# Optimization experiments

Measured on AMD Instinct MI355X. Metric: run time of the kernel, lower is better.

Reference implementation:

```python
import jax, jax.numpy as jnp
import numpy as np

B, NC, D, C, HM = 4096, 32, 128, 256, 2
H = HM * D
EPS = 1e-5


def _ln(x, g, b):
    mu = jnp.mean(x, axis=-1, keepdims=True)
    var = jnp.mean(jnp.square(x - mu), axis=-1, keepdims=True)
    return (x - mu) * jax.lax.rsqrt(var + EPS) * g + b


def setup_inputs() -> dict:
    key = jax.random.key(0)
    ks = jax.random.split(key, 16)
    s = 0.05
    return {
        "cx": jax.random.normal(ks[0], (B, 16), jnp.float32),
        "cat_vecs": jax.random.normal(ks[1], (B, NC, D), jnp.float32),
        "embed_weights": jax.random.normal(ks[2], (NC, C, D), jnp.float32),
        "Wq": jax.random.normal(ks[3], (NC, D, D), jnp.float32) * s,
        "Wk": jax.random.normal(ks[4], (NC, D, D), jnp.float32) * s,
        "Wv": jax.random.normal(ks[5], (NC, D, D), jnp.float32) * s,
        "ln1_g": jnp.ones((D,), jnp.float32),
        "ln1_b": jnp.zeros((D,), jnp.float32),
        "W1": jax.random.normal(ks[6], (NC, D, H), jnp.float32) * s,
        "b1": jnp.zeros((NC, H), jnp.float32),
        "W2": jax.random.normal(ks[7], (NC, H, D), jnp.float32) * s,
        "b2": jnp.zeros((NC, D), jnp.float32),
        "ln2_g": jnp.ones((D,), jnp.float32),
        "ln2_b": jnp.zeros((D,), jnp.float32),
        "Ws": jax.random.normal(ks[8], (NC, D), jnp.float32) * s,
        "bs": jnp.zeros((NC,), jnp.float32),
    }


def reference(cx, cat_vecs, embed_weights, Wq, Wk, Wv, ln1_g, ln1_b, W1, b1, W2, b2, ln2_g, ln2_b, Ws, bs):
    # cx is unused by the original forward body.
    # Per-feature projections, batched over the Nc axis (j).
    q = jnp.einsum('bjd,jde->bje', cat_vecs, Wq)          # [B, Nc, D]
    k = jnp.einsum('jcd,jde->jce', embed_weights, Wk)     # [Nc, C, D]
    v = jnp.einsum('jcd,jde->jce', embed_weights, Wv)     # [Nc, C, D]
    scores = jnp.einsum('bjd,jcd->bjc', q, k) / jnp.sqrt(jnp.asarray(D, q.dtype))
    alpha = jax.nn.softmax(scores, axis=-1)               # [B, Nc, C]
    h = jnp.einsum('bjc,jcd->bjd', alpha, v)              # [B, Nc, D]
    h = _ln(cat_vecs + h, ln1_g, ln1_b)
    ff = jnp.einsum('bjd,jdh->bjh', h, W1) + b1
    ff = jnp.einsum('bjh,jhd->bjd', jax.nn.relu(ff), W2) + b2
    h = _ln(h + ff, ln2_g, ln2_b)
    out = jax.nn.sigmoid(jnp.einsum('bjd,jd->bj', h, Ws) + bs)  # [B, Nc]
    return out
```

## Files before the change

kernel.cpp:

```cpp
#include <hip/hip_runtime.h>


typedef __attribute__((ext_vector_type(4))) float f32x4;
typedef __attribute__((ext_vector_type(8))) short bf16x8;
typedef __attribute__((ext_vector_type(4))) unsigned u32x4;

#define DEVI static __device__ __forceinline__
#define SB __builtin_amdgcn_sched_barrier(0)
#define BARR __builtin_amdgcn_s_barrier()
#define MEMF asm volatile("" ::: "memory")

constexpr int NC = 32, D = 128, C = 256, H = 256;

DEVI unsigned short f2b(float f) {
  unsigned u = __builtin_bit_cast(unsigned, f);
  u += 0x7fffu + ((u >> 16) & 1u);
  return (unsigned short)(u >> 16);
}
DEVI float b2f(unsigned short h) {
  unsigned u = ((unsigned)h) << 16;
  return __builtin_bit_cast(float, u);
}
DEVI unsigned pk2(float a, float b) {
  return (unsigned)f2b(a) | ((unsigned)f2b(b) << 16);
}
DEVI unsigned cvtpk(float a, float b) {
  unsigned r;
  asm("v_cvt_pk_bf16_f32 %0, %1, %2" : "=v"(r) : "v"(a), "v"(b));
  return r;
}

template <int N> DEVI void vmwait() {
  asm volatile("s_waitcnt vmcnt(%0)" ::"n"(N) : "memory");
}
DEVI void lgkm0() { asm volatile("s_waitcnt lgkmcnt(0)" ::: "memory"); }

DEVI void gload16(const void* g, void* l) {
  __builtin_amdgcn_global_load_lds(
      (const __attribute__((address_space(1))) void*)g,
      (__attribute__((address_space(3))) void*)l, 16, 0, 0);
}


__global__ __launch_bounds__(256) void prepA_kernel(
    const float* __restrict__ emb, const float* __restrict__ Wk,
    const float* __restrict__ Wv, const float* __restrict__ W1,
    const float* __restrict__ W2, float* __restrict__ Ktmp,
    unsigned short* __restrict__ VtP, unsigned short* __restrict__ W1tP,
    unsigned short* __restrict__ W2tP) {
  __shared__ __align__(16) float smem[20480];
  const int bid = blockIdx.x, tid = threadIdx.x;
  if (bid < 512) {
    const bool isV = bid >= 256;
    const int bb = isV ? bid - 256 : bid;
    const int j = bb >> 3, ct = bb & 7;
    float* wm = smem;
    float* eb = smem + 16384;
    const float4* gw = (const float4*)((isV ? Wv : Wk) + (long)j * D * D);
    float4* lw = (float4*)wm;
    for (int i = tid; i < D * D / 4; i += 256) lw[i] = gw[i];
    const float4* ge = (const float4*)(emb + ((long)j * C + ct * 32) * D);
    float4* le = (float4*)eb;
    for (int i = tid; i < 32 * D / 4; i += 256) le[i] = ge[i];
    __syncthreads();
    const int e = tid & 127, h = tid >> 7;
    float acc[16];
#pragma unroll
    for (int r = 0; r < 16; ++r) acc[r] = 0.f;
    for (int d = 0; d < D; ++d) {
      float wde = wm[d * 128 + e];
#pragma unroll
      for (int r = 0; r < 16; ++r)
        acc[r] = fmaf(eb[(h * 16 + r) * 128 + d], wde, acc[r]);
    }
    if (!isV) {
      for (int r = 0; r < 16; ++r)
        Ktmp[((long)j * C + ct * 32 + h * 16 + r) * D + e] = acc[r];
    } else {
#pragma unroll
      for (int k = 0; k < 2; ++k) {
        uint4 pk = {pk2(acc[k * 8 + 0], acc[k * 8 + 1]),
                    pk2(acc[k * 8 + 2], acc[k * 8 + 3]),
                    pk2(acc[k * 8 + 4], acc[k * 8 + 5]),
                    pk2(acc[k * 8 + 6], acc[k * 8 + 7])};
        int slot = ct * 4 + h * 2 + k;
        long byte = (long)j * 65536 + e * 512 + ((slot ^ (e & 7)) << 4);
        *(uint4*)((char*)VtP + byte) = pk;
      }
    }
  } else {
    float(*t)[33] = reinterpret_cast<float(*)[33]>(smem);
    const int idx = bid - 512;
    const bool isW2 = idx >= 1024;
    const int bb = isW2 ? idx - 1024 : idx;
    const int j = bb >> 5, tile = bb & 31;
    const int rr = tid >> 3, c4 = tid & 7;
    if (!isW2) {
      const int dt = tile & 3, ht = tile >> 2;
      float4 v = *(const float4*)(W1 + ((long)j * 128 + dt * 32 + rr) * 256 + ht * 32 + c4 * 4);
      t[rr][c4 * 4 + 0] = v.x; t[rr][c4 * 4 + 1] = v.y;
      t[rr][c4 * 4 + 2] = v.z; t[rr][c4 * 4 + 3] = v.w;
      __syncthreads();
      int row = ht * 32 + rr, colb = dt * 32 + c4 * 4;
      uint2 pk = {pk2(t[c4 * 4 + 0][rr], t[c4 * 4 + 1][rr]),
                  pk2(t[c4 * 4 + 2][rr], t[c4 * 4 + 3][rr])};
      long byte = (long)j * 65536 + row * 256 + (((colb >> 3) ^ (row & 7)) << 4) + (colb & 7) * 2;
      *(uint2*)((char*)W1tP + byte) = pk;
    } else {
      const int et = tile & 3, ht = tile >> 2;
      float4 v = *(const float4*)(W2 + ((long)j * 256 + ht * 32 + rr) * 128 + et * 32 + c4 * 4);
      t[rr][c4 * 4 + 0] = v.x; t[rr][c4 * 4 + 1] = v.y;
      t[rr][c4 * 4 + 2] = v.z; t[rr][c4 * 4 + 3] = v.w;
      __syncthreads();
      int row = et * 32 + rr, colb = ht * 32 + c4 * 4;
      uint2 pk = {pk2(t[c4 * 4 + 0][rr], t[c4 * 4 + 1][rr]),
                  pk2(t[c4 * 4 + 2][rr], t[c4 * 4 + 3][rr])};
      long byte = (long)j * 65536 + row * 512 + (((colb >> 3) ^ (row & 7)) << 4) + (colb & 7) * 2;
      *(uint2*)((char*)W2tP + byte) = pk;
    }
  }
}

__global__ __launch_bounds__(256) void prepB_kernel(
    const float* __restrict__ Wq, const float* __restrict__ Ktmp,
    unsigned short* __restrict__ MtP) {
  __shared__ float wqT[128][68];
  __shared__ float kt[32][129];
  const int bid = blockIdx.x;
  const int j = bid >> 4, ct = (bid >> 1) & 7, dh = bid & 1;
  const int tid = threadIdx.x;
  for (int i = tid; i < 64 * 32; i += 256) {
    int dloc = i >> 5, e4 = i & 31;
    float4 v = *(const float4*)(Wq + ((long)j * 128 + dh * 64 + dloc) * 128 + e4 * 4);
    wqT[e4 * 4 + 0][dloc] = v.x; wqT[e4 * 4 + 1][dloc] = v.y;
    wqT[e4 * 4 + 2][dloc] = v.z; wqT[e4 * 4 + 3][dloc] = v.w;
  }
  for (int i = tid; i < 32 * 32; i += 256) {
    int r = i >> 5, c0 = (i & 31) * 4;
    float4 v = *(const float4*)(Ktmp + ((long)j * 256 + ct * 32 + r) * 128 + c0);
    kt[r][c0 + 0] = v.x; kt[r][c0 + 1] = v.y;
    kt[r][c0 + 2] = v.z; kt[r][c0 + 3] = v.w;
  }
  __syncthreads();
  const int cl = tid >> 3, s = tid & 7;
  float acc[8];
#pragma unroll
  for (int u = 0; u < 8; ++u) acc[u] = 0.f;
  for (int e = 0; e < 128; ++e) {
    float kk = kt[cl][e];
    float4 a = *(const float4*)&wqT[e][s * 8];
    float4 b = *(const float4*)&wqT[e][s * 8 + 4];
    acc[0] = fmaf(a.x, kk, acc[0]); acc[1] = fmaf(a.y, kk, acc[1]);
    acc[2] = fmaf(a.z, kk, acc[2]); acc[3] = fmaf(a.w, kk, acc[3]);
    acc[4] = fmaf(b.x, kk, acc[4]); acc[5] = fmaf(b.y, kk, acc[5]);
    acc[6] = fmaf(b.z, kk, acc[6]); acc[7] = fmaf(b.w, kk, acc[7]);
  }
  const float scale = 0.08838834764831845f;
  int c = ct * 32 + cl;
  uint4 pk = {pk2(acc[0] * scale, acc[1] * scale),
              pk2(acc[2] * scale, acc[3] * scale),
              pk2(acc[4] * scale, acc[5] * scale),
              pk2(acc[6] * scale, acc[7] * scale)};
  int slot = dh * 8 + s;
  long byte = (long)j * 65536 + c * 256 + ((slot ^ (c & 7)) << 4);
  *(uint4*)((char*)MtP + byte) = pk;
}

__global__ __launch_bounds__(256, 4) void fused_kernel(
    const float* __restrict__ x, const unsigned short* __restrict__ MtP,
    const unsigned short* __restrict__ VtP, const unsigned short* __restrict__ W1tP,
    const unsigned short* __restrict__ W2tP, const float* __restrict__ b1,
    const float* __restrict__ b2, const float* __restrict__ g1,
    const float* __restrict__ be1, const float* __restrict__ g2,
    const float* __restrict__ be2, const float* __restrict__ Ws,
    const float* __restrict__ bs, float* __restrict__ out) {
  __shared__ __align__(16) unsigned short wb[2][8192];
  __shared__ __align__(16) float sv[1024];
  const int bid = blockIdx.x;
  const int wg = (bid & 7) * 256 + (bid >> 3);
  const int j = wg >> 6, b0 = (wg & 63) * 64;
  const int tid = threadIdx.x, w = tid >> 6, l = tid & 63, lr = l & 15, lg = l >> 4;
  const int bloc = w * 16 + lr;

  const unsigned short* pnl0 = MtP + (long)j * 32768;
  const unsigned short* pnl1 = VtP + (long)j * 32768;
  const unsigned short* pnl2 = W1tP + (long)j * 32768;
  const unsigned short* pnl3 = W2tP + (long)j * 32768;

  auto ISSUE = [&](int s2) {
    const unsigned short* base = (s2 < 4) ? pnl0 : (s2 < 8) ? pnl1 : (s2 < 12) ? pnl2 : pnl3;
    const char* gq = (const char*)(base + (s2 & 3) * 8192);
    char* lb = (char*)&wb[s2 & 1][0] + w * 4096;
    SB;
#pragma unroll
    for (int t = 0; t < 4; ++t)
      gload16(gq + (w * 4 + t) * 1024 + l * 16, lb + t * 1024);
    SB;
  };

  const float* xrow = x + ((long)(b0 + bloc) * NC + j) * D;
  float4 xf[4][2];
#pragma unroll
  for (int kc = 0; kc < 4; ++kc) {
    xf[kc][0] = *(const float4*)(xrow + kc * 32 + lg * 8);
    xf[kc][1] = *(const float4*)(xrow + kc * 32 + lg * 8 + 4);
  }
  for (int i = tid; i < 1024; i += 256) {
    float v;
    if (i < 256) v = b1[j * H + i];
    else if (i < 384) v = b2[j * D + i - 256];
    else if (i < 512) v = g1[i - 384];
    else if (i < 640) v = be1[i - 512];
    else if (i < 768) v = g2[i - 640];
    else if (i < 896) v = be2[i - 768];
    else v = Ws[j * D + i - 896];
    sv[i] = v;
  }
  SB;
  ISSUE(0);
  ISSUE(1);
  float bsj = bs[j];
  bf16x8 xa[4];
#pragma unroll
  for (int kc = 0; kc < 4; ++kc) {
    u32x4 t;
    t[0] = cvtpk(xf[kc][0].x, xf[kc][0].y);
    t[1] = cvtpk(xf[kc][0].z, xf[kc][0].w);
    t[2] = cvtpk(xf[kc][1].x, xf[kc][1].y);
    t[3] = cvtpk(xf[kc][1].z, xf[kc][1].w);
    xa[kc] = __builtin_bit_cast(bf16x8, t);
  }
  lgkm0(); SB; BARR; MEMF; SB;

  int inner[4], inner2[8];
#pragma unroll
  for (int kc = 0; kc < 4; ++kc)
    inner[kc] = lr * 256 + (((kc * 4 + lg) ^ (lr & 7)) << 4);
#pragma unroll
  for (int kc = 0; kc < 8; ++kc)
    inner2[kc] = lr * 512 + (((kc * 4 + lg) ^ (lr & 7)) << 4);

  const int ad0 = (((lg & 1) << 5) + lr) << 2;
  const int ad1 = ad0 + 64;
  const bool hi = (lg >> 1) != 0;

  bf16x8 aa[8], xa2[4], aa2[8];
  unsigned hb[8][2];
  float4 xr[8];

  f32x4 sc[16];
#pragma unroll
  for (int t = 0; t < 16; ++t) sc[t] = (f32x4){0.f, 0.f, 0.f, 0.f};
#pragma unroll
  for (int q = 0; q < 4; ++q) {
    vmwait<4>(); SB; BARR; MEMF; SB;
    const char* wp = (const char*)wb[q & 1];
    __builtin_amdgcn_s_setprio(1);
#pragma unroll
    for (int c4 = 0; c4 < 4; ++c4)
#pragma unroll
      for (int kc = 0; kc < 4; ++kc) {
        bf16x8 bf = *(const bf16x8*)(wp + c4 * 4096 + inner[kc]);
        sc[q * 4 + c4] =
            __builtin_amdgcn_mfma_f32_16x16x32_bf16(bf, xa[kc], sc[q * 4 + c4], 0, 0, 0);
      }
    __builtin_amdgcn_s_setprio(0);
    if (q == 3) {
      float mx = -1e30f;
#pragma unroll
      for (int ct = 0; ct < 16; ++ct)
#pragma unroll
        for (int i = 0; i < 4; ++i) mx = fmaxf(mx, sc[ct][i]);
      mx = fmaxf(mx, __shfl_xor(mx, 16));
      mx = fmaxf(mx, __shfl_xor(mx, 32));
      float sm = 0.f;
#pragma unroll
      for (int ct = 0; ct < 16; ++ct)
#pragma unroll
        for (int i = 0; i < 4; ++i) {
          float e = __expf(sc[ct][i] - mx);
          sc[ct][i] = e;
          sm += e;
        }
      sm += __shfl_xor(sm, 16);
      sm += __shfl_xor(sm, 32);
      float inv = 1.f / sm;
      unsigned au[16][2];
#pragma unroll
      for (int ct = 0; ct < 16; ++ct) {
        au[ct][0] = cvtpk(sc[ct][0] * inv, sc[ct][1] * inv);
        au[ct][1] = cvtpk(sc[ct][2] * inv, sc[ct][3] * inv);
      }
#pragma unroll
      for (int kc = 0; kc < 8; ++kc) {
        u32x4 t;
#pragma unroll
        for (int h = 0; h < 2; ++h) {
          int ad = h ? ad1 : ad0;
#pragma unroll
          for (int p = 0; p < 2; ++p) {
            int f0 = __builtin_amdgcn_ds_bpermute(ad, (int)au[2 * kc][p]);
            int f1 = __builtin_amdgcn_ds_bpermute(ad, (int)au[2 * kc + 1][p]);
            t[h * 2 + p] = (unsigned)(hi ? f1 : f0);
          }
        }
        aa[kc] = __builtin_bit_cast(bf16x8, t);
      }
    }
    lgkm0(); SB; BARR; MEMF; SB;
    ISSUE(q + 2);
  }

  f32x4 ha[8];
#pragma unroll
  for (int t = 0; t < 8; ++t) ha[t] = (f32x4){0.f, 0.f, 0.f, 0.f};
#pragma unroll
  for (int q = 0; q < 4; ++q) {
    vmwait<4>(); SB; BARR; MEMF; SB;
    const char* wp = (const char*)wb[q & 1];
    __builtin_amdgcn_s_setprio(1);
#pragma unroll
    for (int e2 = 0; e2 < 2; ++e2)
#pragma unroll
      for (int kc = 0; kc < 8; ++kc) {
        bf16x8 bf = *(const bf16x8*)(wp + e2 * 8192 + inner2[kc]);
        ha[q * 2 + e2] =
            __builtin_amdgcn_mfma_f32_16x16x32_bf16(bf, aa[kc], ha[q * 2 + e2], 0, 0, 0);
      }
    __builtin_amdgcn_s_setprio(0);
    if (q == 2) {
#pragma unroll
      for (int et = 0; et < 8; ++et)
        xr[et] = *(const float4*)(xrow + et * 16 + lg * 4);
    }
    if (q == 3) {
      float hvv[8][4];
      float s1 = 0.f, s2s = 0.f;
#pragma unroll
      for (int et = 0; et < 8; ++et)
#pragma unroll
        for (int i = 0; i < 4; ++i) {
          float v = ha[et][i] + xr[et][i];
          hvv[et][i] = v;
          s1 += v;
          s2s += v * v;
        }
      s1 += __shfl_xor(s1, 16); s2s += __shfl_xor(s2s, 16);
      s1 += __shfl_xor(s1, 32); s2s += __shfl_xor(s2s, 32);
      float mu = s1 * (1.f / 128.f);
      float var = s2s * (1.f / 128.f) - mu * mu;
      float rs = rsqrtf(var + 1e-5f);
#pragma unroll
      for (int et = 0; et < 8; ++et) {
        f32x4 gg = *(const f32x4*)&sv[384 + et * 16 + lg * 4];
        f32x4 bb = *(const f32x4*)&sv[512 + et * 16 + lg * 4];
        float h0 = (hvv[et][0] - mu) * rs * gg[0] + bb[0];
        float h1n = (hvv[et][1] - mu) * rs * gg[1] + bb[1];
        float h2 = (hvv[et][2] - mu) * rs * gg[2] + bb[2];
        float h3 = (hvv[et][3] - mu) * rs * gg[3] + bb[3];
        hb[et][0] = cvtpk(h0, h1n);
        hb[et][1] = cvtpk(h2, h3);
      }
#pragma unroll
      for (int kc = 0; kc < 4; ++kc) {
        u32x4 t;
#pragma unroll
        for (int h = 0; h < 2; ++h) {
          int ad = h ? ad1 : ad0;
#pragma unroll
          for (int p = 0; p < 2; ++p) {
            int f0 = __builtin_amdgcn_ds_bpermute(ad, (int)hb[2 * kc][p]);
            int f1 = __builtin_amdgcn_ds_bpermute(ad, (int)hb[2 * kc + 1][p]);
            t[h * 2 + p] = (unsigned)(hi ? f1 : f0);
          }
        }
        xa2[kc] = __builtin_bit_cast(bf16x8, t);
      }
    }
    lgkm0(); SB; BARR; MEMF; SB;
    ISSUE(6 + q);
  }

  unsigned ffu[16][2];
#pragma unroll
  for (int q = 0; q < 4; ++q) {
    vmwait<4>(); SB; BARR; MEMF; SB;
    const char* wp = (const char*)wb[q & 1];
    f32x4 fa4[4];
#pragma unroll
    for (int t = 0; t < 4; ++t) fa4[t] = (f32x4){0.f, 0.f, 0.f, 0.f};
    __builtin_amdgcn_s_setprio(1);
#pragma unroll
    for (int c4 = 0; c4 < 4; ++c4)
#pragma unroll
      for (int kc = 0; kc < 4; ++kc) {
        bf16x8 bf = *(const bf16x8*)(wp + c4 * 4096 + inner[kc]);
        fa4[c4] =
            __builtin_amdgcn_mfma_f32_16x16x32_bf16(bf, xa2[kc], fa4[c4], 0, 0, 0);
      }
    __builtin_amdgcn_s_setprio(0);
#pragma unroll
    for (int c4 = 0; c4 < 4; ++c4) {
      int ht = q * 4 + c4;
      f32x4 bb = *(const f32x4*)&sv[ht * 16 + lg * 4];
      float v0 = fmaxf(fa4[c4][0] + bb[0], 0.f);
      float v1 = fmaxf(fa4[c4][1] + bb[1], 0.f);
      float v2 = fmaxf(fa4[c4][2] + bb[2], 0.f);
      float v3 = fmaxf(fa4[c4][3] + bb[3], 0.f);
      ffu[ht][0] = cvtpk(v0, v1);
      ffu[ht][1] = cvtpk(v2, v3);
    }
    if (q == 3) {
#pragma unroll
      for (int kc = 0; kc < 8; ++kc) {
        u32x4 t;
#pragma unroll
        for (int h = 0; h < 2; ++h) {
          int ad = h ? ad1 : ad0;
#pragma unroll
          for (int p = 0; p < 2; ++p) {
            int f0 = __builtin_amdgcn_ds_bpermute(ad, (int)ffu[2 * kc][p]);
            int f1 = __builtin_amdgcn_ds_bpermute(ad, (int)ffu[2 * kc + 1][p]);
            t[h * 2 + p] = (unsigned)(hi ? f1 : f0);
          }
        }
        aa2[kc] = __builtin_bit_cast(bf16x8, t);
      }
    }
    lgkm0(); SB; BARR; MEMF; SB;
    ISSUE(10 + q);
  }

  f32x4 oa[8];
#pragma unroll
  for (int t = 0; t < 8; ++t) oa[t] = (f32x4){0.f, 0.f, 0.f, 0.f};
#pragma unroll
  for (int q = 0; q < 4; ++q) {
    if (q == 3) { vmwait<0>(); } else { vmwait<4>(); }
    SB; BARR; MEMF; SB;
    const char* wp = (const char*)wb[q & 1];
    __builtin_amdgcn_s_setprio(1);
#pragma unroll
    for (int e2 = 0; e2 < 2; ++e2)
#pragma unroll
      for (int kc = 0; kc < 8; ++kc) {
        bf16x8 bf = *(const bf16x8*)(wp + e2 * 8192 + inner2[kc]);
        oa[q * 2 + e2] =
            __builtin_amdgcn_mfma_f32_16x16x32_bf16(bf, aa2[kc], oa[q * 2 + e2], 0, 0, 0);
      }
    __builtin_amdgcn_s_setprio(0);
    if (q < 3) {
      lgkm0(); SB; BARR; MEMF; SB;
      if (q < 2) ISSUE(14 + q);
    }
  }
  {
    float t1 = 0.f, t2 = 0.f;
#pragma unroll
    for (int et = 0; et < 8; ++et) {
      f32x4 bb = *(const f32x4*)&sv[256 + et * 16 + lg * 4];
      float r0 = b2f((unsigned short)(hb[et][0] & 0xffff));
      float r1 = b2f((unsigned short)(hb[et][0] >> 16));
      float r2 = b2f((unsigned short)(hb[et][1] & 0xffff));
      float r3 = b2f((unsigned short)(hb[et][1] >> 16));
      float v0 = oa[et][0] + bb[0] + r0;
      float v1 = oa[et][1] + bb[1] + r1;
      float v2 = oa[et][2] + bb[2] + r2;
      float v3 = oa[et][3] + bb[3] + r3;
      oa[et][0] = v0; oa[et][1] = v1; oa[et][2] = v2; oa[et][3] = v3;
      t1 += (v0 + v1) + (v2 + v3);
      t2 += (v0 * v0 + v1 * v1) + (v2 * v2 + v3 * v3);
    }
    t1 += __shfl_xor(t1, 16); t2 += __shfl_xor(t2, 16);
    t1 += __shfl_xor(t1, 32); t2 += __shfl_xor(t2, 32);
    float mu2 = t1 * (1.f / 128.f);
    float var = t2 * (1.f / 128.f) - mu2 * mu2;
    float rs2 = rsqrtf(var + 1e-5f);
    float lp = 0.f;
#pragma unroll
    for (int et = 0; et < 8; ++et) {
      f32x4 gg = *(const f32x4*)&sv[640 + et * 16 + lg * 4];
      f32x4 bb = *(const f32x4*)&sv[768 + et * 16 + lg * 4];
      f32x4 ww = *(const f32x4*)&sv[896 + et * 16 + lg * 4];
#pragma unroll
      for (int i = 0; i < 4; ++i) {
        float h2 = (oa[et][i] - mu2) * rs2 * gg[i] + bb[i];
        lp = fmaf(h2, ww[i], lp);
      }
    }
    lp += __shfl_xor(lp, 16);
    lp += __shfl_xor(lp, 32);
    if (lg == 0) {
      float sg = 1.f / (1.f + __expf(-(lp + bsj)));
      out[(long)(b0 + bloc) * NC + j] = sg;
    }
  }
}

extern "C" void kernel_launch(void* const* d_in, const int* in_sizes, int n_in,
                              void* d_out, int out_size, void* d_ws,
                              size_t ws_size, hipStream_t stream) {
  (void)in_sizes; (void)n_in; (void)out_size; (void)ws_size;
  const float* cat = (const float*)d_in[1];
  const float* emb = (const float*)d_in[2];
  const float* Wq = (const float*)d_in[3];
  const float* Wk = (const float*)d_in[4];
  const float* Wv = (const float*)d_in[5];
  const float* g1 = (const float*)d_in[6];
  const float* be1 = (const float*)d_in[7];
  const float* W1 = (const float*)d_in[8];
  const float* b1 = (const float*)d_in[9];
  const float* W2 = (const float*)d_in[10];
  const float* b2 = (const float*)d_in[11];
  const float* g2 = (const float*)d_in[12];
  const float* be2 = (const float*)d_in[13];
  const float* Ws = (const float*)d_in[14];
  const float* bs = (const float*)d_in[15];
  float* out = (float*)d_out;

  char* ws = (char*)d_ws;
  unsigned short* MtP = (unsigned short*)(ws);
  unsigned short* VtP = (unsigned short*)(ws + (2 << 20));
  unsigned short* W1tP = (unsigned short*)(ws + (4 << 20));
  unsigned short* W2tP = (unsigned short*)(ws + (6 << 20));
  float* Ktmp = (float*)(ws + (8 << 20));

  prepA_kernel<<<2560, 256, 0, stream>>>(emb, Wk, Wv, W1, W2, Ktmp, VtP, W1tP, W2tP);
  prepB_kernel<<<512, 256, 0, stream>>>(Wq, Ktmp, MtP);
  fused_kernel<<<2048, 256, 0, stream>>>(cat, MtP, VtP, W1tP, W2tP, b1, b2, g1,
                                         be1, g2, be2, Ws, bs, out);
}
```

Baseline: 114.3 us.

## Process two 64-row batch tiles per workgroup with continuous weight prefetch

Each workgroup now handles 128 batch rows for one feature j, as two sequential 64-row tiles, and the grid is halved. The weight-panel prefetch stream keeps running across the tile boundary, so the second tile's first panels load during the first tile's tail. This amortises launch and prologue cost and pipeline fill/drain per panel stream. The trade-off is fewer workgroups, which can reduce occupancy and load balance, and a serial dependency between the two tiles.

```diff
diff --git a/kernel.cpp b/kernel.cpp
--- a/kernel.cpp
+++ b/kernel.cpp
@@ -177,8 +177,8 @@
   __shared__ __align__(16) unsigned short wb[2][8192];
   __shared__ __align__(16) float sv[1024];
   const int bid = blockIdx.x;
-  const int wg = (bid & 7) * 256 + (bid >> 3);
-  const int j = wg >> 6, b0 = (wg & 63) * 64;
+  const int wg = (bid & 7) * 128 + (bid >> 3);
+  const int j = wg >> 5, bpair = wg & 31;
   const int tid = threadIdx.x, w = tid >> 6, l = tid & 63, lr = l & 15, lg = l >> 4;
   const int bloc = w * 16 + lr;
 
@@ -187,10 +187,11 @@
   const unsigned short* pnl2 = W1tP + (long)j * 32768;
   const unsigned short* pnl3 = W2tP + (long)j * 32768;
 
-  auto ISSUE = [&](int s2) {
-    const unsigned short* base = (s2 < 4) ? pnl0 : (s2 < 8) ? pnl1 : (s2 < 12) ? pnl2 : pnl3;
-    const char* gq = (const char*)(base + (s2 & 3) * 8192);
-    char* lb = (char*)&wb[s2 & 1][0] + w * 4096;
+  auto ISSUE = [&](int g) {
+    const int qq = g & 15;
+    const unsigned short* base = (qq < 4) ? pnl0 : (qq < 8) ? pnl1 : (qq < 12) ? pnl2 : pnl3;
+    const char* gq = (const char*)(base + (qq & 3) * 8192);
+    char* lb = (char*)&wb[g & 1][0] + w * 4096;
     SB;
 #pragma unroll
     for (int t = 0; t < 4; ++t)
@@ -198,7 +199,7 @@
     SB;
   };
 
-  const float* xrow = x + ((long)(b0 + bloc) * NC + j) * D;
+  const float* xrow = x + ((long)(bpair * 128 + bloc) * NC + j) * D;
   float4 xf[4][2];
 #pragma unroll
   for (int kc = 0; kc < 4; ++kc) {
@@ -244,255 +245,279 @@
   const int ad1 = ad0 + 64;
   const bool hi = (lg >> 1) != 0;
 
-  bf16x8 aa[8], xa2[4], aa2[8];
-  unsigned hb[8][2];
-  float4 xr[8];
-
-  f32x4 sc[16];
-#pragma unroll
-  for (int t = 0; t < 16; ++t) sc[t] = (f32x4){0.f, 0.f, 0.f, 0.f};
-#pragma unroll
-  for (int q = 0; q < 4; ++q) {
-    vmwait<4>(); SB; BARR; MEMF; SB;
-    const char* wp = (const char*)wb[q & 1];
-    __builtin_amdgcn_s_setprio(1);
-#pragma unroll
-    for (int c4 = 0; c4 < 4; ++c4)
+  for (int bt = 0; bt < 2; ++bt) {
+    const int b0 = bpair * 128 + bt * 64;
+    if (bt == 1) {
+      xrow = x + ((long)(b0 + bloc) * NC + j) * D;
 #pragma unroll
       for (int kc = 0; kc < 4; ++kc) {
-        bf16x8 bf = *(const bf16x8*)(wp + c4 * 4096 + inner[kc]);
-        sc[q * 4 + c4] =
-            __builtin_amdgcn_mfma_f32_16x16x32_bf16(bf, xa[kc], sc[q * 4 + c4], 0, 0, 0);
-      }
-    __builtin_amdgcn_s_setprio(0);
-    if (q == 3) {
-      float mx = -1e30f;
-#pragma unroll
-      for (int ct = 0; ct < 16; ++ct)
-#pragma unroll
-        for (int i = 0; i < 4; ++i) mx = fmaxf(mx, sc[ct][i]);
-      mx = fmaxf(mx, __shfl_xor(mx, 16));
-      mx = fmaxf(mx, __shfl_xor(mx, 32));
-      float sm = 0.f;
-#pragma unroll
-      for (int ct = 0; ct < 16; ++ct)
-#pragma unroll
-        for (int i = 0; i < 4; ++i) {
-          float e = __expf(sc[ct][i] - mx);
-          sc[ct][i] = e;
-          sm += e;
-        }
-      sm += __shfl_xor(sm, 16);
-      sm += __shfl_xor(sm, 32);
-      float inv = 1.f / sm;
-      unsigned au[16][2];
-#pragma unroll
-      for (int ct = 0; ct < 16; ++ct) {
-        au[ct][0] = cvtpk(sc[ct][0] * inv, sc[ct][1] * inv);
-        au[ct][1] = cvtpk(sc[ct][2] * inv, sc[ct][3] * inv);
-      }
-#pragma unroll
-      for (int kc = 0; kc < 8; ++kc) {
-        u32x4 t;
-#pragma unroll
-        for (int h = 0; h < 2; ++h) {
-          int ad = h ? ad1 : ad0;
-#pragma unroll
-          for (int p = 0; p < 2; ++p) {
-            int f0 = __builtin_amdgcn_ds_bpermute(ad, (int)au[2 * kc][p]);
-            int f1 = __builtin_amdgcn_ds_bpermute(ad, (int)au[2 * kc + 1][p]);
-            t[h * 2 + p] = (unsigned)(hi ? f1 : f0);
-          }
-        }
-        aa[kc] = __builtin_bit_cast(bf16x8, t);
-      }
-    }
-    lgkm0(); SB; BARR; MEMF; SB;
-    ISSUE(q + 2);
-  }
-
-  f32x4 ha[8];
-#pragma unroll
-  for (int t = 0; t < 8; ++t) ha[t] = (f32x4){0.f, 0.f, 0.f, 0.f};
-#pragma unroll
-  for (int q = 0; q < 4; ++q) {
-    vmwait<4>(); SB; BARR; MEMF; SB;
-    const char* wp = (const char*)wb[q & 1];
-    __builtin_amdgcn_s_setprio(1);
-#pragma unroll
-    for (int e2 = 0; e2 < 2; ++e2)
-#pragma unroll
-      for (int kc = 0; kc < 8; ++kc) {
-        bf16x8 bf = *(const bf16x8*)(wp + e2 * 8192 + inner2[kc]);
-        ha[q * 2 + e2] =
-            __builtin_amdgcn_mfma_f32_16x16x32_bf16(bf, aa[kc], ha[q * 2 + e2], 0, 0, 0);
-      }
-    __builtin_amdgcn_s_setprio(0);
-    if (q == 2) {
-#pragma unroll
-      for (int et = 0; et < 8; ++et)
-        xr[et] = *(const float4*)(xrow + et * 16 + lg * 4);
-    }
-    if (q == 3) {
-      float hvv[8][4];
-      float s1 = 0.f, s2s = 0.f;
-#pragma unroll
-      for (int et = 0; et < 8; ++et)
-#pragma unroll
-        for (int i = 0; i < 4; ++i) {
-          float v = ha[et][i] + xr[et][i];
-          hvv[et][i] = v;
-          s1 += v;
-          s2s += v * v;
-        }
-      s1 += __shfl_xor(s1, 16); s2s += __shfl_xor(s2s, 16);
-      s1 += __shfl_xor(s1, 32); s2s += __shfl_xor(s2s, 32);
-      float mu = s1 * (1.f / 128.f);
-      float var = s2s * (1.f / 128.f) - mu * mu;
-      float rs = rsqrtf(var + 1e-5f);
-#pragma unroll
-      for (int et = 0; et < 8; ++et) {
-        f32x4 gg = *(const f32x4*)&sv[384 + et * 16 + lg * 4];
-        f32x4 bb = *(const f32x4*)&sv[512 + et * 16 + lg * 4];
-        float h0 = (hvv[et][0] - mu) * rs * gg[0] + bb[0];
-        float h1n = (hvv[et][1] - mu) * rs * gg[1] + bb[1];
-        float h2 = (hvv[et][2] - mu) * rs * gg[2] + bb[2];
-        float h3 = (hvv[et][3] - mu) * rs * gg[3] + bb[3];
-        hb[et][0] = cvtpk(h0, h1n);
-        hb[et][1] = cvtpk(h2, h3);
-      }
+        xf[kc][0] = *(const float4*)(xrow + kc * 32 + lg * 8);
+        xf[kc][1] = *(const float4*)(xrow + kc * 32 + lg * 8 + 4);
+      }
+      vmwait<0>(); SB;
 #pragma unroll
       for (int kc = 0; kc < 4; ++kc) {
         u32x4 t;
-#pragma unroll
-        for (int h = 0; h < 2; ++h) {
-          int ad = h ? ad1 : ad0;
-#pragma unroll
-          for (int p = 0; p < 2; ++p) {
-            int f0 = __builtin_amdgcn_ds_bpermute(ad, (int)hb[2 * kc][p]);
-            int f1 = __builtin_amdgcn_ds_bpermute(ad, (int)hb[2 * kc + 1][p]);
-            t[h * 2 + p] = (unsigned)(hi ? f1 : f0);
+        t[0] = cvtpk(xf[kc][0].x, xf[kc][0].y);
+        t[1] = cvtpk(xf[kc][0].z, xf[kc][0].w);
+        t[2] = cvtpk(xf[kc][1].x, xf[kc][1].y);
+        t[3] = cvtpk(xf[kc][1].z, xf[kc][1].w);
+        xa[kc] = __builtin_bit_cast(bf16x8, t);
+      }
+    }
+    const int gb = bt * 16;
+
+    bf16x8 aa[8], xa2[4], aa2[8];
+    unsigned hb[8][2];
+    float4 xr[8];
+
+    f32x4 sc[16];
+#pragma unroll
+    for (int t = 0; t < 16; ++t) sc[t] = (f32x4){0.f, 0.f, 0.f, 0.f};
+#pragma unroll
+    for (int q = 0; q < 4; ++q) {
+      vmwait<4>(); SB; BARR; MEMF; SB;
+      const char* wp = (const char*)wb[q & 1];
+      __builtin_amdgcn_s_setprio(1);
+#pragma unroll
+      for (int c4 = 0; c4 < 4; ++c4)
+#pragma unroll
+        for (int kc = 0; kc < 4; ++kc) {
+          bf16x8 bf = *(const bf16x8*)(wp + c4 * 4096 + inner[kc]);
+          sc[q * 4 + c4] =
+              __builtin_amdgcn_mfma_f32_16x16x32_bf16(bf, xa[kc], sc[q * 4 + c4], 0, 0, 0);
+        }
+      __builtin_amdgcn_s_setprio(0);
+      if (q == 3) {
+        float mx = -1e30f;
+#pragma unroll
+        for (int ct = 0; ct < 16; ++ct)
+#pragma unroll
+          for (int i = 0; i < 4; ++i) mx = fmaxf(mx, sc[ct][i]);
+        mx = fmaxf(mx, __shfl_xor(mx, 16));
+        mx = fmaxf(mx, __shfl_xor(mx, 32));
+        float sm = 0.f;
+#pragma unroll
+        for (int ct = 0; ct < 16; ++ct)
+#pragma unroll
+          for (int i = 0; i < 4; ++i) {
+            float e = __expf(sc[ct][i] - mx);
+            sc[ct][i] = e;
+            sm += e;
           }
-        }
-        xa2[kc] = __builtin_bit_cast(bf16x8, t);
-      }
-    }
-    lgkm0(); SB; BARR; MEMF; SB;
-    ISSUE(6 + q);
-  }
-
-  unsigned ffu[16][2];
-#pragma unroll
-  for (int q = 0; q < 4; ++q) {
-    vmwait<4>(); SB; BARR; MEMF; SB;
-    const char* wp = (const char*)wb[q & 1];
-    f32x4 fa4[4];
-#pragma unroll
-    for (int t = 0; t < 4; ++t) fa4[t] = (f32x4){0.f, 0.f, 0.f, 0.f};
-    __builtin_amdgcn_s_setprio(1);
-#pragma unroll
-    for (int c4 = 0; c4 < 4; ++c4)
-#pragma unroll
-      for (int kc = 0; kc < 4; ++kc) {
-        bf16x8 bf = *(const bf16x8*)(wp + c4 * 4096 + inner[kc]);
-        fa4[c4] =
-            __builtin_amdgcn_mfma_f32_16x16x32_bf16(bf, xa2[kc], fa4[c4], 0, 0, 0);
-      }
-    __builtin_amdgcn_s_setprio(0);
-#pragma unroll
-    for (int c4 = 0; c4 < 4; ++c4) {
-      int ht = q * 4 + c4;
-      f32x4 bb = *(const f32x4*)&sv[ht * 16 + lg * 4];
-      float v0 = fmaxf(fa4[c4][0] + bb[0], 0.f);
-      float v1 = fmaxf(fa4[c4][1] + bb[1], 0.f);
-      float v2 = fmaxf(fa4[c4][2] + bb[2], 0.f);
-      float v3 = fmaxf(fa4[c4][3] + bb[3], 0.f);
-      ffu[ht][0] = cvtpk(v0, v1);
-      ffu[ht][1] = cvtpk(v2, v3);
-    }
-    if (q == 3) {
-#pragma unroll
-      for (int kc = 0; kc < 8; ++kc) {
-        u32x4 t;
-#pragma unroll
-        for (int h = 0; h < 2; ++h) {
-          int ad = h ? ad1 : ad0;
-#pragma unroll
-          for (int p = 0; p < 2; ++p) {
-            int f0 = __builtin_amdgcn_ds_bpermute(ad, (int)ffu[2 * kc][p]);
-            int f1 = __builtin_amdgcn_ds_bpermute(ad, (int)ffu[2 * kc + 1][p]);
-            t[h * 2 + p] = (unsigned)(hi ? f1 : f0);
+        sm += __shfl_xor(sm, 16);
+        sm += __shfl_xor(sm, 32);
+        float inv = 1.f / sm;
+        unsigned au[16][2];
+#pragma unroll
+        for (int ct = 0; ct < 16; ++ct) {
+          au[ct][0] = cvtpk(sc[ct][0] * inv, sc[ct][1] * inv);
+          au[ct][1] = cvtpk(sc[ct][2] * inv, sc[ct][3] * inv);
+        }
+#pragma unroll
+        for (int kc = 0; kc < 8; ++kc) {
+          u32x4 t;
+#pragma unroll
+          for (int h = 0; h < 2; ++h) {
+            int ad = h ? ad1 : ad0;
+#pragma unroll
+            for (int p = 0; p < 2; ++p) {
+              int f0 = __builtin_amdgcn_ds_bpermute(ad, (int)au[2 * kc][p]);
+              int f1 = __builtin_amdgcn_ds_bpermute(ad, (int)au[2 * kc + 1][p]);
+              t[h * 2 + p] = (unsigned)(hi ? f1 : f0);
+            }
           }
-        }
-        aa2[kc] = __builtin_bit_cast(bf16x8, t);
-      }
-    }
-    lgkm0(); SB; BARR; MEMF; SB;
-    ISSUE(10 + q);
-  }
-
-  f32x4 oa[8];
-#pragma unroll
-  for (int t = 0; t < 8; ++t) oa[t] = (f32x4){0.f, 0.f, 0.f, 0.f};
-#pragma unroll
-  for (int q = 0; q < 4; ++q) {
-    if (q == 3) { vmwait<0>(); } else { vmwait<4>(); }
-    SB; BARR; MEMF; SB;
-    const char* wp = (const char*)wb[q & 1];
-    __builtin_amdgcn_s_setprio(1);
-#pragma unroll
-    for (int e2 = 0; e2 < 2; ++e2)
-#pragma unroll
-      for (int kc = 0; kc < 8; ++kc) {
-        bf16x8 bf = *(const bf16x8*)(wp + e2 * 8192 + inner2[kc]);
-        oa[q * 2 + e2] =
-            __builtin_amdgcn_mfma_f32_16x16x32_bf16(bf, aa2[kc], oa[q * 2 + e2], 0, 0, 0);
-      }
-    __builtin_amdgcn_s_setprio(0);
-    if (q < 3) {
+          aa[kc] = __builtin_bit_cast(bf16x8, t);
+        }
+      }
       lgkm0(); SB; BARR; MEMF; SB;
-      if (q < 2) ISSUE(14 + q);
-    }
-  }
-  {
-    float t1 = 0.f, t2 = 0.f;
-#pragma unroll
-    for (int et = 0; et < 8; ++et) {
-      f32x4 bb = *(const f32x4*)&sv[256 + et * 16 + lg * 4];
-      float r0 = b2f((unsigned short)(hb[et][0] & 0xffff));
-      float r1 = b2f((unsigned short)(hb[et][0] >> 16));
-      float r2 = b2f((unsigned short)(hb[et][1] & 0xffff));
-      float r3 = b2f((unsigned short)(hb[et][1] >> 16));
-      float v0 = oa[et][0] + bb[0] + r0;
-      float v1 = oa[et][1] + bb[1] + r1;
-      float v2 = oa[et][2] + bb[2] + r2;
-      float v3 = oa[et][3] + bb[3] + r3;
-      oa[et][0] = v0; oa[et][1] = v1; oa[et][2] = v2; oa[et][3] = v3;
-      t1 += (v0 + v1) + (v2 + v3);
-      t2 += (v0 * v0 + v1 * v1) + (v2 * v2 + v3 * v3);
-    }
-    t1 += __shfl_xor(t1, 16); t2 += __shfl_xor(t2, 16);
-    t1 += __shfl_xor(t1, 32); t2 += __shfl_xor(t2, 32);
-    float mu2 = t1 * (1.f / 128.f);
-    float var = t2 * (1.f / 128.f) - mu2 * mu2;
-    float rs2 = rsqrtf(var + 1e-5f);
-    float lp = 0.f;
-#pragma unroll
-    for (int et = 0; et < 8; ++et) {
-      f32x4 gg = *(const f32x4*)&sv[640 + et * 16 + lg * 4];
-      f32x4 bb = *(const f32x4*)&sv[768 + et * 16 + lg * 4];
-      f32x4 ww = *(const f32x4*)&sv[896 + et * 16 + lg * 4];
-#pragma unroll
-      for (int i = 0; i < 4; ++i) {
-        float h2 = (oa[et][i] - mu2) * rs2 * gg[i] + bb[i];
-        lp = fmaf(h2, ww[i], lp);
-      }
-    }
-    lp += __shfl_xor(lp, 16);
-    lp += __shfl_xor(lp, 32);
-    if (lg == 0) {
-      float sg = 1.f / (1.f + __expf(-(lp + bsj)));
-      out[(long)(b0 + bloc) * NC + j] = sg;
+      ISSUE(gb + q + 2);
+    }
+
+    f32x4 ha[8];
+#pragma unroll
+    for (int t = 0; t < 8; ++t) ha[t] = (f32x4){0.f, 0.f, 0.f, 0.f};
+#pragma unroll
+    for (int q = 0; q < 4; ++q) {
+      vmwait<4>(); SB; BARR; MEMF; SB;
+      const char* wp = (const char*)wb[q & 1];
+      __builtin_amdgcn_s_setprio(1);
+#pragma unroll
+      for (int e2 = 0; e2 < 2; ++e2)
+#pragma unroll
+        for (int kc = 0; kc < 8; ++kc) {
+          bf16x8 bf = *(const bf16x8*)(wp + e2 * 8192 + inner2[kc]);
+          ha[q * 2 + e2] =
+              __builtin_amdgcn_mfma_f32_16x16x32_bf16(bf, aa[kc], ha[q * 2 + e2], 0, 0, 0);
+        }
+      __builtin_amdgcn_s_setprio(0);
+      if (q == 2) {
+#pragma unroll
+        for (int et = 0; et < 8; ++et)
+          xr[et] = *(const float4*)(xrow + et * 16 + lg * 4);
+      }
+      if (q == 3) {
+        float hvv[8][4];
+        float s1 = 0.f, s2s = 0.f;
+#pragma unroll
+        for (int et = 0; et < 8; ++et)
+#pragma unroll
+          for (int i = 0; i < 4; ++i) {
+            float v = ha[et][i] + xr[et][i];
+            hvv[et][i] = v;
+            s1 += v;
+            s2s += v * v;
+          }
+        s1 += __shfl_xor(s1, 16); s2s += __shfl_xor(s2s, 16);
+        s1 += __shfl_xor(s1, 32); s2s += __shfl_xor(s2s, 32);
+        float mu = s1 * (1.f / 128.f);
+        float var = s2s * (1.f / 128.f) - mu * mu;
+        float rs = rsqrtf(var + 1e-5f);
+#pragma unroll
+        for (int et = 0; et < 8; ++et) {
+          f32x4 gg = *(const f32x4*)&sv[384 + et * 16 + lg * 4];
+          f32x4 bb = *(const f32x4*)&sv[512 + et * 16 + lg * 4];
+          float h0 = (hvv[et][0] - mu) * rs * gg[0] + bb[0];
+          float h1n = (hvv[et][1] - mu) * rs * gg[1] + bb[1];
+          float h2 = (hvv[et][2] - mu) * rs * gg[2] + bb[2];
+          float h3 = (hvv[et][3] - mu) * rs * gg[3] + bb[3];
+          hb[et][0] = cvtpk(h0, h1n);
+          hb[et][1] = cvtpk(h2, h3);
+        }
+#pragma unroll
+        for (int kc = 0; kc < 4; ++kc) {
+          u32x4 t;
+#pragma unroll
+          for (int h = 0; h < 2; ++h) {
+            int ad = h ? ad1 : ad0;
+#pragma unroll
+            for (int p = 0; p < 2; ++p) {
+              int f0 = __builtin_amdgcn_ds_bpermute(ad, (int)hb[2 * kc][p]);
+              int f1 = __builtin_amdgcn_ds_bpermute(ad, (int)hb[2 * kc + 1][p]);
+              t[h * 2 + p] = (unsigned)(hi ? f1 : f0);
+            }
+          }
+          xa2[kc] = __builtin_bit_cast(bf16x8, t);
+        }
+      }
+      lgkm0(); SB; BARR; MEMF; SB;
+      ISSUE(gb + 6 + q);
+    }
+
+    unsigned ffu[16][2];
+#pragma unroll
+    for (int q = 0; q < 4; ++q) {
+      vmwait<4>(); SB; BARR; MEMF; SB;
+      const char* wp = (const char*)wb[q & 1];
+      f32x4 fa4[4];
+#pragma unroll
+      for (int t = 0; t < 4; ++t) fa4[t] = (f32x4){0.f, 0.f, 0.f, 0.f};
+      __builtin_amdgcn_s_setprio(1);
+#pragma unroll
+      for (int c4 = 0; c4 < 4; ++c4)
+#pragma unroll
+        for (int kc = 0; kc < 4; ++kc) {
+          bf16x8 bf = *(const bf16x8*)(wp + c4 * 4096 + inner[kc]);
+          fa4[c4] =
+              __builtin_amdgcn_mfma_f32_16x16x32_bf16(bf, xa2[kc], fa4[c4], 0, 0, 0);
+        }
+      __builtin_amdgcn_s_setprio(0);
+#pragma unroll
+      for (int c4 = 0; c4 < 4; ++c4) {
+        int ht = q * 4 + c4;
+        f32x4 bb = *(const f32x4*)&sv[ht * 16 + lg * 4];
+        float v0 = fmaxf(fa4[c4][0] + bb[0], 0.f);
+        float v1 = fmaxf(fa4[c4][1] + bb[1], 0.f);
+        float v2 = fmaxf(fa4[c4][2] + bb[2], 0.f);
+        float v3 = fmaxf(fa4[c4][3] + bb[3], 0.f);
+        ffu[ht][0] = cvtpk(v0, v1);
+        ffu[ht][1] = cvtpk(v2, v3);
+      }
+      if (q == 3) {
+#pragma unroll
+        for (int kc = 0; kc < 8; ++kc) {
+          u32x4 t;
+#pragma unroll
+          for (int h = 0; h < 2; ++h) {
+            int ad = h ? ad1 : ad0;
+#pragma unroll
+            for (int p = 0; p < 2; ++p) {
+              int f0 = __builtin_amdgcn_ds_bpermute(ad, (int)ffu[2 * kc][p]);
+              int f1 = __builtin_amdgcn_ds_bpermute(ad, (int)ffu[2 * kc + 1][p]);
+              t[h * 2 + p] = (unsigned)(hi ? f1 : f0);
+            }
+          }
+          aa2[kc] = __builtin_bit_cast(bf16x8, t);
+        }
+      }
+      lgkm0(); SB; BARR; MEMF; SB;
+      ISSUE(gb + 10 + q);
+    }
+
+    f32x4 oa[8];
+#pragma unroll
+    for (int t = 0; t < 8; ++t) oa[t] = (f32x4){0.f, 0.f, 0.f, 0.f};
+#pragma unroll
+    for (int q = 0; q < 4; ++q) {
+      if (bt == 1 && q == 3) { vmwait<0>(); } else { vmwait<4>(); }
+      SB; BARR; MEMF; SB;
+      const char* wp = (const char*)wb[q & 1];
+      __builtin_amdgcn_s_setprio(1);
+#pragma unroll
+      for (int e2 = 0; e2 < 2; ++e2)
+#pragma unroll
+        for (int kc = 0; kc < 8; ++kc) {
+          bf16x8 bf = *(const bf16x8*)(wp + e2 * 8192 + inner2[kc]);
+          oa[q * 2 + e2] =
+              __builtin_amdgcn_mfma_f32_16x16x32_bf16(bf, aa2[kc], oa[q * 2 + e2], 0, 0, 0);
+        }
+      __builtin_amdgcn_s_setprio(0);
+      if (q == 3) {
+        float t1 = 0.f, t2 = 0.f;
+#pragma unroll
+        for (int et = 0; et < 8; ++et) {
+          f32x4 bb = *(const f32x4*)&sv[256 + et * 16 + lg * 4];
+          float r0 = b2f((unsigned short)(hb[et][0] & 0xffff));
+          float r1 = b2f((unsigned short)(hb[et][0] >> 16));
+          float r2 = b2f((unsigned short)(hb[et][1] & 0xffff));
+          float r3 = b2f((unsigned short)(hb[et][1] >> 16));
+          float v0 = oa[et][0] + bb[0] + r0;
+          float v1 = oa[et][1] + bb[1] + r1;
+          float v2 = oa[et][2] + bb[2] + r2;
+          float v3 = oa[et][3] + bb[3] + r3;
+          oa[et][0] = v0; oa[et][1] = v1; oa[et][2] = v2; oa[et][3] = v3;
+          t1 += (v0 + v1) + (v2 + v3);
+          t2 += (v0 * v0 + v1 * v1) + (v2 * v2 + v3 * v3);
+        }
+        t1 += __shfl_xor(t1, 16); t2 += __shfl_xor(t2, 16);
+        t1 += __shfl_xor(t1, 32); t2 += __shfl_xor(t2, 32);
+        float mu2 = t1 * (1.f / 128.f);
+        float var = t2 * (1.f / 128.f) - mu2 * mu2;
+        float rs2 = rsqrtf(var + 1e-5f);
+        float lp = 0.f;
+#pragma unroll
+        for (int et = 0; et < 8; ++et) {
+          f32x4 gg = *(const f32x4*)&sv[640 + et * 16 + lg * 4];
+          f32x4 bb = *(const f32x4*)&sv[768 + et * 16 + lg * 4];
+          f32x4 ww = *(const f32x4*)&sv[896 + et * 16 + lg * 4];
+#pragma unroll
+          for (int i = 0; i < 4; ++i) {
+            float h2 = (oa[et][i] - mu2) * rs2 * gg[i] + bb[i];
+            lp = fmaf(h2, ww[i], lp);
+          }
+        }
+        lp += __shfl_xor(lp, 16);
+        lp += __shfl_xor(lp, 32);
+        if (lg == 0) {
+          float sg = 1.f / (1.f + __expf(-(lp + bsj)));
+          out[(long)(b0 + bloc) * NC + j] = sg;
+        }
+      }
+      const int nxt = gb + 14 + q;
+      if (nxt < 32) {
+        lgkm0(); SB; BARR; MEMF; SB;
+        ISSUE(nxt);
+      }
     }
   }
 }
@@ -527,6 +552,6 @@
 
   prepA_kernel<<<2560, 256, 0, stream>>>(emb, Wk, Wv, W1, W2, Ktmp, VtP, W1tP, W2tP);
   prepB_kernel<<<512, 256, 0, stream>>>(Wq, Ktmp, MtP);
-  fused_kernel<<<2048, 256, 0, stream>>>(cat, MtP, VtP, W1tP, W2tP, b1, b2, g1,
+  fused_kernel<<<1024, 256, 0, stream>>>(cat, MtP, VtP, W1tP, W2tP, b1, b2, g1,
                                          be1, g2, be2, Ws, bs, out);
 }
```

Result: slower. 179.5 us (+57.0%).

## Precompute Wk·Wq^T per feature so prep computes scaled keys directly

Applied to the files above, without the earlier changes.

Reassociates the key-query product: a small new kernel computes G = Wk·Wq^T per feature (128x128). The embedding prep then multiplies emb by G and writes the scaled bf16 M matrix in its swizzled layout directly. This removes the fp32 Ktmp round trip and the separate prepB pass over 256 keys. It adds a small dependent launch, and the M stores become scattered 2-byte writes instead of 16-byte packed ones.

```diff
diff --git a/kernel.cpp b/kernel.cpp
--- a/kernel.cpp
+++ b/kernel.cpp
@@ -42,10 +42,53 @@
 }
 
 
+__global__ __launch_bounds__(256) void prepG_kernel(
+    const float* __restrict__ Wk, const float* __restrict__ Wq,
+    float* __restrict__ G) {
+  __shared__ float wqT[128][132];
+  __shared__ float wkb[32][132];
+  const int j = blockIdx.x >> 2, ft = blockIdx.x & 3;
+  const int tid = threadIdx.x;
+  for (int i = tid; i < 128 * 32; i += 256) {
+    int d = i >> 5, e4 = i & 31;
+    float4 v = *(const float4*)(Wq + ((long)j * 128 + d) * 128 + e4 * 4);
+    wqT[e4 * 4 + 0][d] = v.x; wqT[e4 * 4 + 1][d] = v.y;
+    wqT[e4 * 4 + 2][d] = v.z; wqT[e4 * 4 + 3][d] = v.w;
+  }
+  for (int i = tid; i < 32 * 32; i += 256) {
+    int r = i >> 5, e0 = (i & 31) * 4;
+    float4 v = *(const float4*)(Wk + ((long)j * 128 + ft * 32 + r) * 128 + e0);
+    wkb[r][e0] = v.x; wkb[r][e0 + 1] = v.y;
+    wkb[r][e0 + 2] = v.z; wkb[r][e0 + 3] = v.w;
+  }
+  __syncthreads();
+  const int fl = tid >> 3, s = tid & 7;
+  float acc[16];
+#pragma unroll
+  for (int u = 0; u < 16; ++u) acc[u] = 0.f;
+  for (int e = 0; e < 128; ++e) {
+    float kk = wkb[fl][e];
+#pragma unroll
+    for (int u4 = 0; u4 < 4; ++u4) {
+      float4 a = *(const float4*)&wqT[e][s * 16 + u4 * 4];
+      acc[u4 * 4 + 0] = fmaf(a.x, kk, acc[u4 * 4 + 0]);
+      acc[u4 * 4 + 1] = fmaf(a.y, kk, acc[u4 * 4 + 1]);
+      acc[u4 * 4 + 2] = fmaf(a.z, kk, acc[u4 * 4 + 2]);
+      acc[u4 * 4 + 3] = fmaf(a.w, kk, acc[u4 * 4 + 3]);
+    }
+  }
+  float* gout = G + (long)j * 16384 + (ft * 32 + fl) * 128 + s * 16;
+#pragma unroll
+  for (int u4 = 0; u4 < 4; ++u4) {
+    float4 v = {acc[u4 * 4 + 0], acc[u4 * 4 + 1], acc[u4 * 4 + 2], acc[u4 * 4 + 3]};
+    *(float4*)(gout + u4 * 4) = v;
+  }
+}
+
 __global__ __launch_bounds__(256) void prepA_kernel(
-    const float* __restrict__ emb, const float* __restrict__ Wk,
+    const float* __restrict__ emb, const float* __restrict__ G,
     const float* __restrict__ Wv, const float* __restrict__ W1,
-    const float* __restrict__ W2, float* __restrict__ Ktmp,
+    const float* __restrict__ W2, unsigned short* __restrict__ MtP,
     unsigned short* __restrict__ VtP, unsigned short* __restrict__ W1tP,
     unsigned short* __restrict__ W2tP) {
   __shared__ __align__(16) float smem[20480];
@@ -56,7 +99,7 @@
     const int j = bb >> 3, ct = bb & 7;
     float* wm = smem;
     float* eb = smem + 16384;
-    const float4* gw = (const float4*)((isV ? Wv : Wk) + (long)j * D * D);
+    const float4* gw = (const float4*)((isV ? Wv : G) + (long)j * D * D);
     float4* lw = (float4*)wm;
     for (int i = tid; i < D * D / 4; i += 256) lw[i] = gw[i];
     const float4* ge = (const float4*)(emb + ((long)j * C + ct * 32) * D);
@@ -74,8 +117,13 @@
         acc[r] = fmaf(eb[(h * 16 + r) * 128 + d], wde, acc[r]);
     }
     if (!isV) {
-      for (int r = 0; r < 16; ++r)
-        Ktmp[((long)j * C + ct * 32 + h * 16 + r) * D + e] = acc[r];
+      const float scale = 0.08838834764831845f;
+#pragma unroll
+      for (int r = 0; r < 16; ++r) {
+        int c = ct * 32 + h * 16 + r;
+        long byte = (long)j * 65536 + c * 256 + (((e >> 3) ^ (c & 7)) << 4) + (e & 7) * 2;
+        *(unsigned short*)((char*)MtP + byte) = f2b(acc[r] * scale);
+      }
     } else {
 #pragma unroll
       for (int k = 0; k < 2; ++k) {
@@ -121,51 +169,6 @@
   }
 }
 
-__global__ __launch_bounds__(256) void prepB_kernel(
-    const float* __restrict__ Wq, const float* __restrict__ Ktmp,
-    unsigned short* __restrict__ MtP) {
-  __shared__ float wqT[128][68];
-  __shared__ float kt[32][129];
-  const int bid = blockIdx.x;
-  const int j = bid >> 4, ct = (bid >> 1) & 7, dh = bid & 1;
-  const int tid = threadIdx.x;
-  for (int i = tid; i < 64 * 32; i += 256) {
-    int dloc = i >> 5, e4 = i & 31;
-    float4 v = *(const float4*)(Wq + ((long)j * 128 + dh * 64 + dloc) * 128 + e4 * 4);
-    wqT[e4 * 4 + 0][dloc] = v.x; wqT[e4 * 4 + 1][dloc] = v.y;
-    wqT[e4 * 4 + 2][dloc] = v.z; wqT[e4 * 4 + 3][dloc] = v.w;
-  }
-  for (int i = tid; i < 32 * 32; i += 256) {
-    int r = i >> 5, c0 = (i & 31) * 4;
-    float4 v = *(const float4*)(Ktmp + ((long)j * 256 + ct * 32 + r) * 128 + c0);
-    kt[r][c0 + 0] = v.x; kt[r][c0 + 1] = v.y;
-    kt[r][c0 + 2] = v.z; kt[r][c0 + 3] = v.w;
-  }
-  __syncthreads();
-  const int cl = tid >> 3, s = tid & 7;
-  float acc[8];
-#pragma unroll
-  for (int u = 0; u < 8; ++u) acc[u] = 0.f;
-  for (int e = 0; e < 128; ++e) {
-    float kk = kt[cl][e];
-    float4 a = *(const float4*)&wqT[e][s * 8];
-    float4 b = *(const float4*)&wqT[e][s * 8 + 4];
-    acc[0] = fmaf(a.x, kk, acc[0]); acc[1] = fmaf(a.y, kk, acc[1]);
-    acc[2] = fmaf(a.z, kk, acc[2]); acc[3] = fmaf(a.w, kk, acc[3]);
-    acc[4] = fmaf(b.x, kk, acc[4]); acc[5] = fmaf(b.y, kk, acc[5]);
-    acc[6] = fmaf(b.z, kk, acc[6]); acc[7] = fmaf(b.w, kk, acc[7]);
-  }
-  const float scale = 0.08838834764831845f;
-  int c = ct * 32 + cl;
-  uint4 pk = {pk2(acc[0] * scale, acc[1] * scale),
-              pk2(acc[2] * scale, acc[3] * scale),
-              pk2(acc[4] * scale, acc[5] * scale),
-              pk2(acc[6] * scale, acc[7] * scale)};
-  int slot = dh * 8 + s;
-  long byte = (long)j * 65536 + c * 256 + ((slot ^ (c & 7)) << 4);
-  *(uint4*)((char*)MtP + byte) = pk;
-}
-
 __global__ __launch_bounds__(256, 4) void fused_kernel(
     const float* __restrict__ x, const unsigned short* __restrict__ MtP,
     const unsigned short* __restrict__ VtP, const unsigned short* __restrict__ W1tP,
@@ -523,10 +526,10 @@
   unsigned short* VtP = (unsigned short*)(ws + (2 << 20));
   unsigned short* W1tP = (unsigned short*)(ws + (4 << 20));
   unsigned short* W2tP = (unsigned short*)(ws + (6 << 20));
-  float* Ktmp = (float*)(ws + (8 << 20));
-
-  prepA_kernel<<<2560, 256, 0, stream>>>(emb, Wk, Wv, W1, W2, Ktmp, VtP, W1tP, W2tP);
-  prepB_kernel<<<512, 256, 0, stream>>>(Wq, Ktmp, MtP);
+  float* G = (float*)(ws + (8 << 20));
+
+  prepG_kernel<<<128, 256, 0, stream>>>(Wk, Wq, G);
+  prepA_kernel<<<2560, 256, 0, stream>>>(emb, G, Wv, W1, W2, MtP, VtP, W1tP, W2tP);
   fused_kernel<<<2048, 256, 0, stream>>>(cat, MtP, VtP, W1tP, W2tP, b1, b2, g1,
                                          be1, g2, be2, Ws, bs, out);
 }
```

Measured after the change: 115.9 us. No clear change (+1.3%).
